# Performance work log

Measured on AMD Instinct MI355X. Metric: run time of the kernel, lower is better.

## Reference

```python
import jax, jax.numpy as jnp
import numpy as np

EPS = 1e-5


def _gn(v, axes, gamma, beta):
    # GroupNorm: normalize over `axes` per (batch, group), then affine.
    mu = jnp.mean(v, axis=axes, keepdims=True)
    var = jnp.var(v, axis=axes, keepdims=True)
    return (v - mu) * jax.lax.rsqrt(var + EPS) * gamma + beta


def setup_inputs() -> dict:
    key = jax.random.key(0)
    ks = jax.random.split(key, 5)
    B, G, BW, S, CD, H = 8, 32, 64, 64, 256, 64
    x = jax.random.normal(ks[0], (B, G * BW, H, H), jnp.float32)
    sent_embs = jax.random.normal(ks[1], (B, CD), jnp.float32)
    # grouped 1x1 conv weights stored as [group, out_per_group, in_per_group]
    Wq = jax.random.normal(ks[2], (G, S, CD), jnp.float32) * 0.05
    Wk = jax.random.normal(ks[3], (G, S, BW), jnp.float32) * 0.05
    Wv = jax.random.normal(ks[4], (G, S, BW), jnp.float32) * 0.05
    gamma1 = jnp.ones((G * S,), jnp.float32)
    beta1 = jnp.zeros((G * S,), jnp.float32)
    gamma2 = jnp.ones((G * S,), jnp.float32)
    beta2 = jnp.zeros((G * S,), jnp.float32)
    return {"x": x, "sent_embs": sent_embs, "Wq": Wq, "Wk": Wk, "Wv": Wv,
            "gamma1": gamma1, "beta1": beta1, "gamma2": gamma2, "beta2": beta2}


def reference(x, sent_embs, Wq, Wk, Wv, gamma1, beta1, gamma2, beta2):
    G, S, CD = Wq.shape
    B, C, H, W = x.shape
    BW = C // G
    xr = x.reshape(B, G, BW, H * W)                    # [B,G,bw,N]
    # query: same sent_emb broadcast to every group, grouped 1x1 conv
    q = jnp.einsum('bc,gsc->bgs', sent_embs, Wq)       # [B,G,S]
    q = _gn(q, (2,), gamma1.reshape(G, S), beta1.reshape(G, S))
    # key: grouped 1x1 conv over spatial map
    k = jnp.einsum('bgcn,gsc->bgsn', xr, Wk)           # [B,G,S,N]
    k = _gn(k, (2, 3), gamma2.reshape(G, S, 1), beta2.reshape(G, S, 1))
    # single-query attention per (batch, group)
    sim = jnp.einsum('bgs,bgsn->bgn', q, k)            # [B,G,N]
    attn = jax.nn.softmax(sim, axis=-1)
    out = jnp.einsum('bgn,bgcn->bgc', attn, xr)        # [B,G,bw]
    out = jnp.einsum('bgc,gsc->bgs', out, Wv)          # value grouped conv
    return out.reshape(B, G * S, 1, 1)
```

## Files before the change

### kernel.cpp

```cpp
#include <hip/hip_runtime.h>
#include <stdint.h>


#define EPS 1e-5f
#define NN 4096
#define NCHUNK 16
#define NSTR 264

typedef __bf16 bf16x8 __attribute__((ext_vector_type(8)));
typedef float f32x4 __attribute__((ext_vector_type(4)));

__global__ __launch_bounds__(64) void kA(const float* __restrict__ sent,
                                         const float* __restrict__ Wq,
                                         const float* __restrict__ Wk,
                                         const float* __restrict__ g1,
                                         const float* __restrict__ b1,
                                         const float* __restrict__ g2,
                                         float* __restrict__ w_all) {
  int bg = blockIdx.x; int b = bg >> 5; int g = bg & 31;
  int t = threadIdx.x;
  const float* wqrow = Wq + (size_t)(g * 64 + t) * 256;
  const float* se = sent + b * 256;
  float q = 0.f;
  for (int c = 0; c < 256; c += 4) {
    float4 wv = *(const float4*)(wqrow + c);
    q += se[c] * wv.x + se[c + 1] * wv.y + se[c + 2] * wv.z + se[c + 3] * wv.w;
  }
  float s = q;
  for (int off = 32; off; off >>= 1) s += __shfl_xor(s, off);
  float mu = s * (1.f / 64.f);
  float d = q - mu;
  float v = d * d;
  for (int off = 32; off; off >>= 1) v += __shfl_xor(v, off);
  float rsq = rsqrtf(v * (1.f / 64.f) + EPS);
  int gs = g * 64 + t;
  float qg2 = (d * rsq * g1[gs] + b1[gs]) * g2[gs];
  __shared__ float qs[64];
  qs[t] = qg2;
  __syncthreads();
  float wacc = 0.f;
  for (int s2 = 0; s2 < 64; s2++)
    wacc += qs[s2] * Wk[(size_t)(g * 64 + s2) * 64 + t];
  w_all[bg * 64 + t] = wacc;
}

__global__ __launch_bounds__(256) void kM(const float* __restrict__ Wk,
                                          float4* __restrict__ Mp,
                                          float* __restrict__ cw) {
  int g = blockIdx.x; int t = threadIdx.x;
  __shared__ float wk[4096];
  __shared__ float Ml[64 * 65];
  const float* wg = Wk + (size_t)g * 4096;
  #pragma unroll
  for (int i = 0; i < 16; i++) wk[t + 256 * i] = wg[t + 256 * i];
  __syncthreads();
  int c = t & 63, q = t >> 6;
  float acc[16];
  #pragma unroll
  for (int i = 0; i < 16; i++) acc[i] = 0.f;
  for (int s = 0; s < 64; s++) {
    float a = wk[s * 64 + c];
    const float* r = &wk[s * 64 + q * 16];
    #pragma unroll
    for (int i = 0; i < 16; i++) acc[i] += a * r[i];
  }
  #pragma unroll
  for (int i = 0; i < 16; i++) Ml[(q * 16 + i) * 65 + c] = acc[i];
  float s2 = 0.f;
  if (t < 64) {
    for (int s = 0; s < 64; s++) s2 += wk[s * 64 + t];
  }
  __syncthreads();
  if (t < 64) cw[g * 64 + t] = s2;
  int lane = t & 63, wv = t >> 6;
  int row = wv * 16 + ((lane >> 4) << 2);
  int col = lane & 15;
  #pragma unroll
  for (int r = 0; r < 4; r++) {
    float4 mv;
    mv.x = Ml[(row + 0) * 65 + r * 16 + col];
    mv.y = Ml[(row + 1) * 65 + r * 16 + col];
    mv.z = Ml[(row + 2) * 65 + r * 16 + col];
    mv.w = Ml[(row + 3) * 65 + r * 16 + col];
    Mp[(size_t)(g * 4 + r) * 256 + t] = mv;
  }
}

__global__ __launch_bounds__(256, 4) void kB(const float* __restrict__ x,
                                             const float* __restrict__ w_all,
                                             const float* __restrict__ cw,
                                             const float4* __restrict__ Mp,
                                             float* __restrict__ y_all,
                                             float* __restrict__ sums_part) {
  int bg = blockIdx.y; int b = bg >> 5; int g = bg & 31;
  int n0 = blockIdx.x * 256;
  int t = threadIdx.x;
  int lane = t & 63;
  int wv = t >> 6;

  __shared__ unsigned short xt[64 * NSTR];
  __shared__ float ypart[4 * 256];
  __shared__ float red[8];

  const float* wp = w_all + bg * 64 + wv * 16;
  const float* cwp = cw + g * 64 + wv * 16;
  float4 wq[4], cq[4];
  #pragma unroll
  for (int j = 0; j < 4; j++) { wq[j] = *(const float4*)(wp + j * 4); }
  #pragma unroll
  for (int j = 0; j < 4; j++) { cq[j] = *(const float4*)(cwp + j * 4); }

  const float* xb = x + ((size_t)(b * 2048 + g * 64 + wv * 16)) * NN + n0 + lane * 4;
  float4 v[16];
  #pragma unroll
  for (int k = 0; k < 16; k++) v[k] = *(const float4*)(xb + (size_t)k * NN);

  float y0 = 0, y1 = 0, y2 = 0, y3 = 0, zt = 0;
  unsigned short* xrow = &xt[(wv * 16) * NSTR + lane * 4];
  #pragma unroll
  for (int k = 0; k < 16; k++) {
    float wc = ((const float*)&wq[0])[k];
    float cc = ((const float*)&cq[0])[k];
    float4 vx = v[k];
    y0 += wc * vx.x; y1 += wc * vx.y; y2 += wc * vx.z; y3 += wc * vx.w;
    zt += cc * (vx.x + vx.y + vx.z + vx.w);
    unsigned a0 = __builtin_bit_cast(unsigned, vx.x) + 0x8000u;
    unsigned a1 = __builtin_bit_cast(unsigned, vx.y) + 0x8000u;
    unsigned a2 = __builtin_bit_cast(unsigned, vx.z) + 0x8000u;
    unsigned a3 = __builtin_bit_cast(unsigned, vx.w) + 0x8000u;
    uint2 pk;
    pk.x = (a0 >> 16) | (a1 & 0xffff0000u);
    pk.y = (a2 >> 16) | (a3 & 0xffff0000u);
    *(uint2*)(xrow + k * NSTR) = pk;
  }
  {
    float4 yp; yp.x = y0; yp.y = y1; yp.z = y2; yp.w = y3;
    *(float4*)&ypart[wv * 256 + lane * 4] = yp;
  }
  __syncthreads();
  y_all[(size_t)bg * NN + n0 + t] =
      ypart[t] + ypart[256 + t] + ypart[512 + t] + ypart[768 + t];

  int rbase = (lane & 15) * NSTR;
  int koff = (lane >> 4) * 8;
  int abase = (wv * 16 + (lane & 15)) * NSTR + koff;
  f32x4 acc[4];
  #pragma unroll
  for (int r = 0; r < 4; r++) acc[r] = (f32x4){0.f, 0.f, 0.f, 0.f};
  #pragma unroll
  for (int kk = 0; kk < 8; kk++) {
    uint4 au = *(const uint4*)&xt[abase + kk * 32];
    bf16x8 af = __builtin_bit_cast(bf16x8, au);
    #pragma unroll
    for (int r = 0; r < 4; r++) {
      uint4 bu = *(const uint4*)&xt[r * 16 * NSTR + rbase + kk * 32 + koff];
      bf16x8 bf = __builtin_bit_cast(bf16x8, bu);
      acc[r] = __builtin_amdgcn_mfma_f32_16x16x32_bf16(af, bf, acc[r], 0, 0, 0);
    }
  }
  float s2acc = 0.f;
  {
    const float4* mp = Mp + (size_t)g * 1024 + t;
    #pragma unroll
    for (int r = 0; r < 4; r++) {
      float4 mv = mp[r * 256];
      s2acc += acc[r][0] * mv.x + acc[r][1] * mv.y +
               acc[r][2] * mv.z + acc[r][3] * mv.w;
    }
  }
  for (int off = 32; off; off >>= 1) {
    zt += __shfl_xor(zt, off);
    s2acc += __shfl_xor(s2acc, off);
  }
  if (lane == 0) { red[wv] = zt; red[4 + wv] = s2acc; }
  __syncthreads();
  if (t == 0) {
    float* sp = sums_part + (size_t)(blockIdx.x * 256 + bg) * 2;
    sp[0] = red[0] + red[1] + red[2] + red[3];
    sp[1] = red[4] + red[5] + red[6] + red[7];
  }
}

__global__ __launch_bounds__(256) void kC(const float* __restrict__ y_all,
                                          const float* __restrict__ sums_part,
                                          float* __restrict__ attn) {
  int bg = blockIdx.x; int t = threadIdx.x;
  float s1 = 0.f, s2 = 0.f;
  for (int i = 0; i < NCHUNK; i++) {
    const float* sp = sums_part + (size_t)(i * 256 + bg) * 2;
    s1 += sp[0]; s2 += sp[1];
  }
  float mu = s1 * (1.f / 262144.f);
  float var = s2 * (1.f / 262144.f) - mu * mu;
  float rs = rsqrtf(var + EPS);
  const float* y = y_all + (size_t)bg * NN;
  float l[16];
  float m = -1e30f;
  #pragma unroll
  for (int i = 0; i < 16; i++) {
    l[i] = rs * y[t + 256 * i];
    m = fmaxf(m, l[i]);
  }
  __shared__ float red[8];
  for (int off = 32; off; off >>= 1) m = fmaxf(m, __shfl_xor(m, off));
  int wv = t >> 6, lane = t & 63;
  if (lane == 0) red[wv] = m;
  __syncthreads();
  m = fmaxf(fmaxf(red[0], red[1]), fmaxf(red[2], red[3]));
  float sum = 0.f;
  #pragma unroll
  for (int i = 0; i < 16; i++) { l[i] = __expf(l[i] - m); sum += l[i]; }
  for (int off = 32; off; off >>= 1) sum += __shfl_xor(sum, off);
  if (lane == 0) red[4 + wv] = sum;
  __syncthreads();
  float inv = 1.f / (red[4] + red[5] + red[6] + red[7]);
  float* ao = attn + (size_t)bg * NN;
  #pragma unroll
  for (int i = 0; i < 16; i++) ao[t + 256 * i] = l[i] * inv;
}

__global__ __launch_bounds__(256, 4) void kD(const float* __restrict__ x,
                                             const float* __restrict__ attn,
                                             float* __restrict__ outp) {
  int bg = 255 - blockIdx.y; int b = bg >> 5; int g = bg & 31;
  int n0 = (NCHUNK - 1 - blockIdx.x) * 256;
  int t = threadIdx.x; int lane = t & 63; int wv = t >> 6;
  float4 a = *(const float4*)(attn + (size_t)bg * NN + n0 + lane * 4);
  const float* xb = x + ((size_t)(b * 2048 + g * 64 + wv * 16)) * NN + n0 + lane * 4;
  float4 v[16];
  #pragma unroll
  for (int k = 0; k < 16; k++) v[k] = *(const float4*)(xb + (size_t)k * NN);
  float p[16];
  #pragma unroll
  for (int k = 0; k < 16; k++)
    p[k] = a.x * v[k].x + a.y * v[k].y + a.z * v[k].z + a.w * v[k].w;
  #pragma unroll
  for (int k = 0; k < 16; k++) {
    float r = p[k];
    for (int off = 32; off; off >>= 1) r += __shfl_xor(r, off);
    if (lane == 0)
      outp[(size_t)blockIdx.x * 16384 + bg * 64 + wv * 16 + k] = r;
  }
}

__global__ __launch_bounds__(64) void kE(const float* __restrict__ outp,
                                         const float* __restrict__ Wv,
                                         float* __restrict__ out) {
  int bg = blockIdx.x; int g = bg & 31;
  int t = threadIdx.x;
  __shared__ float oc[64];
  __shared__ float wvs[64 * 65];
  float s = 0.f;
  #pragma unroll
  for (int j = 0; j < NCHUNK; j++) s += outp[j * 16384 + bg * 64 + t];
  oc[t] = s;
  const float* wg = Wv + (size_t)g * 4096;
  for (int i = 0; i < 64; i++) wvs[i * 65 + t] = wg[i * 64 + t];
  __syncthreads();
  float acc = 0.f;
  for (int c = 0; c < 64; c++) acc += wvs[t * 65 + c] * oc[c];
  out[bg * 64 + t] = acc;
}

extern "C" void kernel_launch(void* const* d_in, const int* in_sizes, int n_in,
                              void* d_out, int out_size, void* d_ws, size_t ws_size,
                              hipStream_t stream) {
  const float* x    = (const float*)d_in[0];
  const float* sent = (const float*)d_in[1];
  const float* Wq   = (const float*)d_in[2];
  const float* Wk   = (const float*)d_in[3];
  const float* Wv   = (const float*)d_in[4];
  const float* g1   = (const float*)d_in[5];
  const float* b1   = (const float*)d_in[6];
  const float* g2   = (const float*)d_in[7];
  float* out = (float*)d_out;

  char* ws = (char*)d_ws;
  float*  w_all = (float*)(ws);
  float*  cw    = (float*)(ws + 65536);
  float4* Mp    = (float4*)(ws + 73728);
  float*  sumsp = (float*)(ws + 598016);
  float*  outp  = (float*)(ws + 630784);
  float*  y_all = (float*)(ws + 1679360);
  float*  attn  = (float*)(ws + 5873664);

  kA<<<256, 64, 0, stream>>>(sent, Wq, Wk, g1, b1, g2, w_all);
  kM<<<32, 256, 0, stream>>>(Wk, Mp, cw);
  kB<<<dim3(NCHUNK, 256), 256, 0, stream>>>(x, w_all, cw, Mp, y_all, sumsp);
  kC<<<256, 256, 0, stream>>>(y_all, sumsp, attn);
  kD<<<dim3(NCHUNK, 256), 256, 0, stream>>>(x, attn, outp);
  kE<<<256, 64, 0, stream>>>(outp, Wv, out);
}
```

Baseline: 433.2 us.

## Make kB and kD persistent over half-rows with register double-buffered loads

The streaming kernels kB and kD now launch 512 blocks instead of 4096. Each block walks eight 256-column chunks of half the spatial axis and prefetches the next chunk's x tile into a second register set while it computes the current one. kD walks its chunks in reverse to reuse cache from kB, and kC and kE reduce only two partials. This cuts launch and partial-reduction overhead and hides global load latency. In exchange it doubles register pressure (occupancy hint lowered to 2), adds two block syncs per chunk in kB, and leaves only 512 blocks to fill the GPU.

```diff
diff --git a/kernel.cpp b/kernel.cpp
--- a/kernel.cpp
+++ b/kernel.cpp
@@ -4,7 +4,6 @@
 
 #define EPS 1e-5f
 #define NN 4096
-#define NCHUNK 16
 #define NSTR 264
 
 typedef __bf16 bf16x8 __attribute__((ext_vector_type(8)));
@@ -86,17 +85,16 @@
   }
 }
 
-__global__ __launch_bounds__(256, 4) void kB(const float* __restrict__ x,
+__global__ __launch_bounds__(256, 2) void kB(const float* __restrict__ x,
                                              const float* __restrict__ w_all,
                                              const float* __restrict__ cw,
                                              const float4* __restrict__ Mp,
                                              float* __restrict__ y_all,
                                              float* __restrict__ sums_part) {
-  int bg = blockIdx.y; int b = bg >> 5; int g = bg & 31;
-  int n0 = blockIdx.x * 256;
-  int t = threadIdx.x;
-  int lane = t & 63;
-  int wv = t >> 6;
+  int bid = blockIdx.x;
+  int bg = bid >> 1, half = bid & 1;
+  int b = bg >> 5, g = bg & 31;
+  int t = threadIdx.x, lane = t & 63, wv = t >> 6;
 
   __shared__ unsigned short xt[64 * NSTR];
   __shared__ float ypart[4 * 256];
@@ -104,60 +102,72 @@
 
   const float* wp = w_all + bg * 64 + wv * 16;
   const float* cwp = cw + g * 64 + wv * 16;
-  float4 wq[4], cq[4];
-  #pragma unroll
-  for (int j = 0; j < 4; j++) { wq[j] = *(const float4*)(wp + j * 4); }
-  #pragma unroll
-  for (int j = 0; j < 4; j++) { cq[j] = *(const float4*)(cwp + j * 4); }
-
-  const float* xb = x + ((size_t)(b * 2048 + g * 64 + wv * 16)) * NN + n0 + lane * 4;
-  float4 v[16];
-  #pragma unroll
-  for (int k = 0; k < 16; k++) v[k] = *(const float4*)(xb + (size_t)k * NN);
-
-  float y0 = 0, y1 = 0, y2 = 0, y3 = 0, zt = 0;
+  const float* xb = x + ((size_t)(b * 2048 + g * 64 + wv * 16)) * NN +
+                    half * 2048 + lane * 4;
   unsigned short* xrow = &xt[(wv * 16) * NSTR + lane * 4];
-  #pragma unroll
-  for (int k = 0; k < 16; k++) {
-    float wc = ((const float*)&wq[0])[k];
-    float cc = ((const float*)&cq[0])[k];
-    float4 vx = v[k];
-    y0 += wc * vx.x; y1 += wc * vx.y; y2 += wc * vx.z; y3 += wc * vx.w;
-    zt += cc * (vx.x + vx.y + vx.z + vx.w);
-    unsigned a0 = __builtin_bit_cast(unsigned, vx.x) + 0x8000u;
-    unsigned a1 = __builtin_bit_cast(unsigned, vx.y) + 0x8000u;
-    unsigned a2 = __builtin_bit_cast(unsigned, vx.z) + 0x8000u;
-    unsigned a3 = __builtin_bit_cast(unsigned, vx.w) + 0x8000u;
-    uint2 pk;
-    pk.x = (a0 >> 16) | (a1 & 0xffff0000u);
-    pk.y = (a2 >> 16) | (a3 & 0xffff0000u);
-    *(uint2*)(xrow + k * NSTR) = pk;
-  }
-  {
-    float4 yp; yp.x = y0; yp.y = y1; yp.z = y2; yp.w = y3;
-    *(float4*)&ypart[wv * 256 + lane * 4] = yp;
-  }
-  __syncthreads();
-  y_all[(size_t)bg * NN + n0 + t] =
-      ypart[t] + ypart[256 + t] + ypart[512 + t] + ypart[768 + t];
 
   int rbase = (lane & 15) * NSTR;
   int koff = (lane >> 4) * 8;
   int abase = (wv * 16 + (lane & 15)) * NSTR + koff;
+
+  float zt = 0.f;
   f32x4 acc[4];
   #pragma unroll
   for (int r = 0; r < 4; r++) acc[r] = (f32x4){0.f, 0.f, 0.f, 0.f};
-  #pragma unroll
-  for (int kk = 0; kk < 8; kk++) {
-    uint4 au = *(const uint4*)&xt[abase + kk * 32];
-    bf16x8 af = __builtin_bit_cast(bf16x8, au);
-    #pragma unroll
-    for (int r = 0; r < 4; r++) {
-      uint4 bu = *(const uint4*)&xt[r * 16 * NSTR + rbase + kk * 32 + koff];
-      bf16x8 bf = __builtin_bit_cast(bf16x8, bu);
-      acc[r] = __builtin_amdgcn_mfma_f32_16x16x32_bf16(af, bf, acc[r], 0, 0, 0);
-    }
-  }
+
+  float4 v0[16], v1[16];
+  #pragma unroll
+  for (int k = 0; k < 16; k++) v0[k] = *(const float4*)(xb + (size_t)k * NN);
+
+  auto stepB = [&](int i, float4 (&cur)[16], float4 (&nxt)[16]) {
+    if (i < 7) {
+      const float* xn = xb + (size_t)(i + 1) * 256;
+      #pragma unroll
+      for (int k = 0; k < 16; k++) nxt[k] = *(const float4*)(xn + (size_t)k * NN);
+    }
+    float y0 = 0, y1 = 0, y2 = 0, y3 = 0;
+    uint2 pk[16];
+    #pragma unroll
+    for (int k = 0; k < 16; k++) {
+      float wc = wp[k], cc = cwp[k];
+      float4 vx = cur[k];
+      y0 += wc * vx.x; y1 += wc * vx.y; y2 += wc * vx.z; y3 += wc * vx.w;
+      zt += cc * (vx.x + vx.y + vx.z + vx.w);
+      unsigned a0 = __builtin_bit_cast(unsigned, vx.x) + 0x8000u;
+      unsigned a1 = __builtin_bit_cast(unsigned, vx.y) + 0x8000u;
+      unsigned a2 = __builtin_bit_cast(unsigned, vx.z) + 0x8000u;
+      unsigned a3 = __builtin_bit_cast(unsigned, vx.w) + 0x8000u;
+      pk[k].x = (a0 >> 16) | (a1 & 0xffff0000u);
+      pk[k].y = (a2 >> 16) | (a3 & 0xffff0000u);
+    }
+    __syncthreads();
+    #pragma unroll
+    for (int k = 0; k < 16; k++) *(uint2*)(xrow + k * NSTR) = pk[k];
+    {
+      float4 yp; yp.x = y0; yp.y = y1; yp.z = y2; yp.w = y3;
+      *(float4*)&ypart[wv * 256 + lane * 4] = yp;
+    }
+    __syncthreads();
+    y_all[(size_t)bg * NN + half * 2048 + i * 256 + t] =
+        ypart[t] + ypart[256 + t] + ypart[512 + t] + ypart[768 + t];
+    #pragma unroll
+    for (int kk = 0; kk < 8; kk++) {
+      uint4 au = *(const uint4*)&xt[abase + kk * 32];
+      bf16x8 af = __builtin_bit_cast(bf16x8, au);
+      #pragma unroll
+      for (int r = 0; r < 4; r++) {
+        uint4 bu = *(const uint4*)&xt[r * 16 * NSTR + rbase + kk * 32 + koff];
+        bf16x8 bf = __builtin_bit_cast(bf16x8, bu);
+        acc[r] = __builtin_amdgcn_mfma_f32_16x16x32_bf16(af, bf, acc[r], 0, 0, 0);
+      }
+    }
+  };
+  #pragma unroll
+  for (int ii = 0; ii < 8; ii += 2) {
+    stepB(ii, v0, v1);
+    stepB(ii + 1, v1, v0);
+  }
+
   float s2acc = 0.f;
   {
     const float4* mp = Mp + (size_t)g * 1024 + t;
@@ -175,7 +185,7 @@
   if (lane == 0) { red[wv] = zt; red[4 + wv] = s2acc; }
   __syncthreads();
   if (t == 0) {
-    float* sp = sums_part + (size_t)(blockIdx.x * 256 + bg) * 2;
+    float* sp = sums_part + (size_t)(half * 256 + bg) * 2;
     sp[0] = red[0] + red[1] + red[2] + red[3];
     sp[1] = red[4] + red[5] + red[6] + red[7];
   }
@@ -186,7 +196,7 @@
                                           float* __restrict__ attn) {
   int bg = blockIdx.x; int t = threadIdx.x;
   float s1 = 0.f, s2 = 0.f;
-  for (int i = 0; i < NCHUNK; i++) {
+  for (int i = 0; i < 2; i++) {
     const float* sp = sums_part + (size_t)(i * 256 + bg) * 2;
     s1 += sp[0]; s2 += sp[1];
   }
@@ -219,27 +229,51 @@
   for (int i = 0; i < 16; i++) ao[t + 256 * i] = l[i] * inv;
 }
 
-__global__ __launch_bounds__(256, 4) void kD(const float* __restrict__ x,
+__global__ __launch_bounds__(256, 2) void kD(const float* __restrict__ x,
                                              const float* __restrict__ attn,
                                              float* __restrict__ outp) {
-  int bg = 255 - blockIdx.y; int b = bg >> 5; int g = bg & 31;
-  int n0 = (NCHUNK - 1 - blockIdx.x) * 256;
-  int t = threadIdx.x; int lane = t & 63; int wv = t >> 6;
-  float4 a = *(const float4*)(attn + (size_t)bg * NN + n0 + lane * 4);
-  const float* xb = x + ((size_t)(b * 2048 + g * 64 + wv * 16)) * NN + n0 + lane * 4;
-  float4 v[16];
-  #pragma unroll
-  for (int k = 0; k < 16; k++) v[k] = *(const float4*)(xb + (size_t)k * NN);
+  int bid = blockIdx.x;
+  int bg = bid >> 1, half = bid & 1;
+  int b = bg >> 5, g = bg & 31;
+  int t = threadIdx.x, lane = t & 63, wv = t >> 6;
+  const float* xb = x + ((size_t)(b * 2048 + g * 64 + wv * 16)) * NN +
+                    half * 2048 + lane * 4;
+  const float* ab = attn + (size_t)bg * NN + half * 2048 + lane * 4;
+
   float p[16];
   #pragma unroll
-  for (int k = 0; k < 16; k++)
-    p[k] = a.x * v[k].x + a.y * v[k].y + a.z * v[k].z + a.w * v[k].w;
+  for (int k = 0; k < 16; k++) p[k] = 0.f;
+
+  float4 v0[16], v1[16], a0, a1;
+  {
+    const float* xn = xb + (size_t)7 * 256;
+    a0 = *(const float4*)(ab + 7 * 256);
+    #pragma unroll
+    for (int k = 0; k < 16; k++) v0[k] = *(const float4*)(xn + (size_t)k * NN);
+  }
+  auto stepD = [&](int i, float4 (&cur)[16], float4& ac,
+                   float4 (&nxt)[16], float4& an) {
+    if (i > 0) {
+      const float* xn = xb + (size_t)(i - 1) * 256;
+      an = *(const float4*)(ab + (i - 1) * 256);
+      #pragma unroll
+      for (int k = 0; k < 16; k++) nxt[k] = *(const float4*)(xn + (size_t)k * NN);
+    }
+    #pragma unroll
+    for (int k = 0; k < 16; k++)
+      p[k] += ac.x * cur[k].x + ac.y * cur[k].y +
+              ac.z * cur[k].z + ac.w * cur[k].w;
+  };
+  #pragma unroll
+  for (int ii = 0; ii < 8; ii += 2) {
+    stepD(7 - ii, v0, a0, v1, a1);
+    stepD(6 - ii, v1, a1, v0, a0);
+  }
   #pragma unroll
   for (int k = 0; k < 16; k++) {
     float r = p[k];
     for (int off = 32; off; off >>= 1) r += __shfl_xor(r, off);
-    if (lane == 0)
-      outp[(size_t)blockIdx.x * 16384 + bg * 64 + wv * 16 + k] = r;
+    if (lane == 0) outp[(size_t)half * 16384 + bg * 64 + wv * 16 + k] = r;
   }
 }
 
@@ -250,10 +284,7 @@
   int t = threadIdx.x;
   __shared__ float oc[64];
   __shared__ float wvs[64 * 65];
-  float s = 0.f;
-  #pragma unroll
-  for (int j = 0; j < NCHUNK; j++) s += outp[j * 16384 + bg * 64 + t];
-  oc[t] = s;
+  oc[t] = outp[bg * 64 + t] + outp[16384 + bg * 64 + t];
   const float* wg = Wv + (size_t)g * 4096;
   for (int i = 0; i < 64; i++) wvs[i * 65 + t] = wg[i * 64 + t];
   __syncthreads();
@@ -280,14 +311,14 @@
   float*  cw    = (float*)(ws + 65536);
   float4* Mp    = (float4*)(ws + 73728);
   float*  sumsp = (float*)(ws + 598016);
-  float*  outp  = (float*)(ws + 630784);
-  float*  y_all = (float*)(ws + 1679360);
-  float*  attn  = (float*)(ws + 5873664);
+  float*  outp  = (float*)(ws + 602112);
+  float*  y_all = (float*)(ws + 733184);
+  float*  attn  = (float*)(ws + 4927488);
 
   kA<<<256, 64, 0, stream>>>(sent, Wq, Wk, g1, b1, g2, w_all);
   kM<<<32, 256, 0, stream>>>(Wk, Mp, cw);
-  kB<<<dim3(NCHUNK, 256), 256, 0, stream>>>(x, w_all, cw, Mp, y_all, sumsp);
+  kB<<<512, 256, 0, stream>>>(x, w_all, cw, Mp, y_all, sumsp);
   kC<<<256, 256, 0, stream>>>(y_all, sumsp, attn);
-  kD<<<dim3(NCHUNK, 256), 256, 0, stream>>>(x, attn, outp);
+  kD<<<512, 256, 0, stream>>>(x, attn, outp);
   kE<<<256, 64, 0, stream>>>(outp, Wv, out);
 }
```

New measurement: 531.9 us. 1.23x slower.

## Stage x tiles via direct global-to-LDS loads in kB/kD and widen small kernels

Applied to the files above, without the earlier changes.

kB and kD now copy their 64x256 fp32 x tile straight into shared memory with global_load_lds instead of going through registers. kB computes the y and z projections from shared memory and converts to bf16 on the fly for the MFMA Gram product. kD computes the attention-weighted sums from the shared tile and reduces them in shared memory instead of with 16 shuffle reductions. kA and kE are widened to 256 threads with split-K partial sums. The larger fp32 shared tile lowers occupancy (launch bounds drop to 2 blocks per CU) in exchange for fewer register round trips and shuffles.

```diff
diff --git a/kernel.cpp b/kernel.cpp
--- a/kernel.cpp
+++ b/kernel.cpp
@@ -4,44 +4,75 @@
 
 #define EPS 1e-5f
 #define NN 4096
-#define NCHUNK 16
-#define NSTR 264
+#define XSTR 268
 
 typedef __bf16 bf16x8 __attribute__((ext_vector_type(8)));
 typedef float f32x4 __attribute__((ext_vector_type(4)));
 
-__global__ __launch_bounds__(64) void kA(const float* __restrict__ sent,
-                                         const float* __restrict__ Wq,
-                                         const float* __restrict__ Wk,
-                                         const float* __restrict__ g1,
-                                         const float* __restrict__ b1,
-                                         const float* __restrict__ g2,
-                                         float* __restrict__ w_all) {
+__device__ __forceinline__ void gload16(const float* g, float* l) {
+  __builtin_amdgcn_global_load_lds(
+      (const __attribute__((address_space(1))) unsigned int*)g,
+      (__attribute__((address_space(3))) unsigned int*)l, 16, 0, 0);
+}
+
+__device__ __forceinline__ bf16x8 cvt8(float4 a, float4 b) {
+  unsigned u0 = __builtin_bit_cast(unsigned, a.x) + 0x8000u;
+  unsigned u1 = __builtin_bit_cast(unsigned, a.y) + 0x8000u;
+  unsigned u2 = __builtin_bit_cast(unsigned, a.z) + 0x8000u;
+  unsigned u3 = __builtin_bit_cast(unsigned, a.w) + 0x8000u;
+  unsigned u4 = __builtin_bit_cast(unsigned, b.x) + 0x8000u;
+  unsigned u5 = __builtin_bit_cast(unsigned, b.y) + 0x8000u;
+  unsigned u6 = __builtin_bit_cast(unsigned, b.z) + 0x8000u;
+  unsigned u7 = __builtin_bit_cast(unsigned, b.w) + 0x8000u;
+  uint4 r;
+  r.x = (u0 >> 16) | (u1 & 0xffff0000u);
+  r.y = (u2 >> 16) | (u3 & 0xffff0000u);
+  r.z = (u4 >> 16) | (u5 & 0xffff0000u);
+  r.w = (u6 >> 16) | (u7 & 0xffff0000u);
+  return __builtin_bit_cast(bf16x8, r);
+}
+
+__global__ __launch_bounds__(256) void kA(const float* __restrict__ sent,
+                                          const float* __restrict__ Wq,
+                                          const float* __restrict__ Wk,
+                                          const float* __restrict__ g1,
+                                          const float* __restrict__ b1,
+                                          const float* __restrict__ g2,
+                                          float* __restrict__ w_all) {
   int bg = blockIdx.x; int b = bg >> 5; int g = bg & 31;
-  int t = threadIdx.x;
-  const float* wqrow = Wq + (size_t)(g * 64 + t) * 256;
-  const float* se = sent + b * 256;
-  float q = 0.f;
-  for (int c = 0; c < 256; c += 4) {
-    float4 wv = *(const float4*)(wqrow + c);
-    q += se[c] * wv.x + se[c + 1] * wv.y + se[c + 2] * wv.z + se[c + 3] * wv.w;
-  }
-  float s = q;
-  for (int off = 32; off; off >>= 1) s += __shfl_xor(s, off);
-  float mu = s * (1.f / 64.f);
-  float d = q - mu;
-  float v = d * d;
-  for (int off = 32; off; off >>= 1) v += __shfl_xor(v, off);
-  float rsq = rsqrtf(v * (1.f / 64.f) + EPS);
-  int gs = g * 64 + t;
-  float qg2 = (d * rsq * g1[gs] + b1[gs]) * g2[gs];
-  __shared__ float qs[64];
-  qs[t] = qg2;
-  __syncthreads();
-  float wacc = 0.f;
-  for (int s2 = 0; s2 < 64; s2++)
-    wacc += qs[s2] * Wk[(size_t)(g * 64 + s2) * 64 + t];
-  w_all[bg * 64 + t] = wacc;
+  int t = threadIdx.x, lane = t & 63, wv = t >> 6;
+  __shared__ float qp[256], qs[64], wpp[256];
+  const float* se = sent + b * 256 + wv * 64;
+  const float* wqrow = Wq + (size_t)(g * 64 + lane) * 256 + wv * 64;
+  float acc = 0.f;
+  #pragma unroll
+  for (int c = 0; c < 64; c += 4) {
+    float4 w4 = *(const float4*)(wqrow + c);
+    acc += se[c] * w4.x + se[c + 1] * w4.y + se[c + 2] * w4.z + se[c + 3] * w4.w;
+  }
+  qp[wv * 64 + lane] = acc;
+  __syncthreads();
+  if (wv == 0) {
+    float q = qp[lane] + qp[64 + lane] + qp[128 + lane] + qp[192 + lane];
+    float s = q;
+    for (int off = 32; off; off >>= 1) s += __shfl_xor(s, off);
+    float mu = s * (1.f / 64.f);
+    float d = q - mu;
+    float v = d * d;
+    for (int off = 32; off; off >>= 1) v += __shfl_xor(v, off);
+    float rsq = rsqrtf(v * (1.f / 64.f) + EPS);
+    int gs = g * 64 + lane;
+    qs[lane] = (d * rsq * g1[gs] + b1[gs]) * g2[gs];
+  }
+  __syncthreads();
+  const float* wkb = Wk + (size_t)(g * 64 + wv * 16) * 64 + lane;
+  float wa = 0.f;
+  #pragma unroll
+  for (int s2 = 0; s2 < 16; s2++) wa += qs[wv * 16 + s2] * wkb[s2 * 64];
+  wpp[wv * 64 + lane] = wa;
+  __syncthreads();
+  if (wv == 0)
+    w_all[bg * 64 + lane] = wpp[lane] + wpp[64 + lane] + wpp[128 + lane] + wpp[192 + lane];
 }
 
 __global__ __launch_bounds__(256) void kM(const float* __restrict__ Wk,
@@ -86,76 +117,54 @@
   }
 }
 
-__global__ __launch_bounds__(256, 4) void kB(const float* __restrict__ x,
+__global__ __launch_bounds__(256, 2) void kB(const float* __restrict__ x,
                                              const float* __restrict__ w_all,
                                              const float* __restrict__ cw,
                                              const float4* __restrict__ Mp,
                                              float* __restrict__ y_all,
                                              float* __restrict__ sums_part) {
-  int bg = blockIdx.y; int b = bg >> 5; int g = bg & 31;
-  int n0 = blockIdx.x * 256;
-  int t = threadIdx.x;
-  int lane = t & 63;
-  int wv = t >> 6;
-
-  __shared__ unsigned short xt[64 * NSTR];
-  __shared__ float ypart[4 * 256];
+  int bid = blockIdx.x;
+  int bg = bid >> 4, ch = bid & 15;
+  int b = bg >> 5, g = bg & 31;
+  int t = threadIdx.x, lane = t & 63, wv = t >> 6;
+  int n0 = ch * 256;
+
+  __shared__ float xt[64 * XSTR];
+  __shared__ float wl[64], cwl[64];
   __shared__ float red[8];
 
-  const float* wp = w_all + bg * 64 + wv * 16;
-  const float* cwp = cw + g * 64 + wv * 16;
-  float4 wq[4], cq[4];
-  #pragma unroll
-  for (int j = 0; j < 4; j++) { wq[j] = *(const float4*)(wp + j * 4); }
-  #pragma unroll
-  for (int j = 0; j < 4; j++) { cq[j] = *(const float4*)(cwp + j * 4); }
-
-  const float* xb = x + ((size_t)(b * 2048 + g * 64 + wv * 16)) * NN + n0 + lane * 4;
-  float4 v[16];
-  #pragma unroll
-  for (int k = 0; k < 16; k++) v[k] = *(const float4*)(xb + (size_t)k * NN);
-
-  float y0 = 0, y1 = 0, y2 = 0, y3 = 0, zt = 0;
-  unsigned short* xrow = &xt[(wv * 16) * NSTR + lane * 4];
-  #pragma unroll
-  for (int k = 0; k < 16; k++) {
-    float wc = ((const float*)&wq[0])[k];
-    float cc = ((const float*)&cq[0])[k];
-    float4 vx = v[k];
-    y0 += wc * vx.x; y1 += wc * vx.y; y2 += wc * vx.z; y3 += wc * vx.w;
-    zt += cc * (vx.x + vx.y + vx.z + vx.w);
-    unsigned a0 = __builtin_bit_cast(unsigned, vx.x) + 0x8000u;
-    unsigned a1 = __builtin_bit_cast(unsigned, vx.y) + 0x8000u;
-    unsigned a2 = __builtin_bit_cast(unsigned, vx.z) + 0x8000u;
-    unsigned a3 = __builtin_bit_cast(unsigned, vx.w) + 0x8000u;
-    uint2 pk;
-    pk.x = (a0 >> 16) | (a1 & 0xffff0000u);
-    pk.y = (a2 >> 16) | (a3 & 0xffff0000u);
-    *(uint2*)(xrow + k * NSTR) = pk;
-  }
-  {
-    float4 yp; yp.x = y0; yp.y = y1; yp.z = y2; yp.w = y3;
-    *(float4*)&ypart[wv * 256 + lane * 4] = yp;
-  }
-  __syncthreads();
-  y_all[(size_t)bg * NN + n0 + t] =
-      ypart[t] + ypart[256 + t] + ypart[512 + t] + ypart[768 + t];
-
-  int rbase = (lane & 15) * NSTR;
-  int koff = (lane >> 4) * 8;
-  int abase = (wv * 16 + (lane & 15)) * NSTR + koff;
+  if (t < 64) { wl[t] = w_all[bg * 64 + t]; cwl[t] = cw[g * 64 + t]; }
+
+  const float* xrow = x + ((size_t)(b * 2048 + g * 64 + wv * 16)) * NN + n0 + lane * 4;
+  #pragma unroll
+  for (int k = 0; k < 16; k++)
+    gload16(xrow + (size_t)k * NN, &xt[(wv * 16 + k) * XSTR]);
+  __syncthreads();
+
+  float y = 0.f, z = 0.f;
+  #pragma unroll 8
+  for (int c = 0; c < 64; c++) {
+    float v = xt[c * XSTR + t];
+    y += wl[c] * v;
+    z += cwl[c] * v;
+  }
+  y_all[(size_t)bg * NN + n0 + t] = y;
+
+  int rbase = (lane & 15) * XSTR + (lane >> 4) * 8;
+  int abase = (wv * 16 + (lane & 15)) * XSTR + (lane >> 4) * 8;
   f32x4 acc[4];
   #pragma unroll
   for (int r = 0; r < 4; r++) acc[r] = (f32x4){0.f, 0.f, 0.f, 0.f};
   #pragma unroll
   for (int kk = 0; kk < 8; kk++) {
-    uint4 au = *(const uint4*)&xt[abase + kk * 32];
-    bf16x8 af = __builtin_bit_cast(bf16x8, au);
+    float4 a0 = *(const float4*)&xt[abase + kk * 32];
+    float4 a1 = *(const float4*)&xt[abase + kk * 32 + 4];
+    bf16x8 af = cvt8(a0, a1);
     #pragma unroll
     for (int r = 0; r < 4; r++) {
-      uint4 bu = *(const uint4*)&xt[r * 16 * NSTR + rbase + kk * 32 + koff];
-      bf16x8 bf = __builtin_bit_cast(bf16x8, bu);
-      acc[r] = __builtin_amdgcn_mfma_f32_16x16x32_bf16(af, bf, acc[r], 0, 0, 0);
+      float4 b0 = *(const float4*)&xt[r * 16 * XSTR + rbase + kk * 32];
+      float4 b1 = *(const float4*)&xt[r * 16 * XSTR + rbase + kk * 32 + 4];
+      acc[r] = __builtin_amdgcn_mfma_f32_16x16x32_bf16(af, cvt8(b0, b1), acc[r], 0, 0, 0);
     }
   }
   float s2acc = 0.f;
@@ -169,13 +178,13 @@
     }
   }
   for (int off = 32; off; off >>= 1) {
-    zt += __shfl_xor(zt, off);
+    z += __shfl_xor(z, off);
     s2acc += __shfl_xor(s2acc, off);
   }
-  if (lane == 0) { red[wv] = zt; red[4 + wv] = s2acc; }
+  if (lane == 0) { red[wv] = z; red[4 + wv] = s2acc; }
   __syncthreads();
   if (t == 0) {
-    float* sp = sums_part + (size_t)(blockIdx.x * 256 + bg) * 2;
+    float* sp = sums_part + (size_t)(ch * 256 + bg) * 2;
     sp[0] = red[0] + red[1] + red[2] + red[3];
     sp[1] = red[4] + red[5] + red[6] + red[7];
   }
@@ -186,7 +195,7 @@
                                           float* __restrict__ attn) {
   int bg = blockIdx.x; int t = threadIdx.x;
   float s1 = 0.f, s2 = 0.f;
-  for (int i = 0; i < NCHUNK; i++) {
+  for (int i = 0; i < 16; i++) {
     const float* sp = sums_part + (size_t)(i * 256 + bg) * 2;
     s1 += sp[0]; s2 += sp[1];
   }
@@ -219,47 +228,70 @@
   for (int i = 0; i < 16; i++) ao[t + 256 * i] = l[i] * inv;
 }
 
-__global__ __launch_bounds__(256, 4) void kD(const float* __restrict__ x,
+__global__ __launch_bounds__(256, 2) void kD(const float* __restrict__ x,
                                              const float* __restrict__ attn,
                                              float* __restrict__ outp) {
-  int bg = 255 - blockIdx.y; int b = bg >> 5; int g = bg & 31;
-  int n0 = (NCHUNK - 1 - blockIdx.x) * 256;
-  int t = threadIdx.x; int lane = t & 63; int wv = t >> 6;
-  float4 a = *(const float4*)(attn + (size_t)bg * NN + n0 + lane * 4);
-  const float* xb = x + ((size_t)(b * 2048 + g * 64 + wv * 16)) * NN + n0 + lane * 4;
-  float4 v[16];
-  #pragma unroll
-  for (int k = 0; k < 16; k++) v[k] = *(const float4*)(xb + (size_t)k * NN);
-  float p[16];
+  int bid = blockIdx.x;
+  int bg = 255 - (bid >> 4), ch = 15 - (bid & 15);
+  int b = bg >> 5, g = bg & 31;
+  int t = threadIdx.x, lane = t & 63, wv = t >> 6;
+  int n0 = ch * 256;
+
+  __shared__ float xt[64 * XSTR];
+  __shared__ float al[256];
+  __shared__ float pp[256];
+
+  const float* xrow = x + ((size_t)(b * 2048 + g * 64 + wv * 16)) * NN + n0 + lane * 4;
+  if (wv == 0) gload16(attn + (size_t)bg * NN + n0 + lane * 4, al);
   #pragma unroll
   for (int k = 0; k < 16; k++)
-    p[k] = a.x * v[k].x + a.y * v[k].y + a.z * v[k].z + a.w * v[k].w;
-  #pragma unroll
-  for (int k = 0; k < 16; k++) {
-    float r = p[k];
-    for (int off = 32; off; off >>= 1) r += __shfl_xor(r, off);
-    if (lane == 0)
-      outp[(size_t)blockIdx.x * 16384 + bg * 64 + wv * 16 + k] = r;
-  }
-}
-
-__global__ __launch_bounds__(64) void kE(const float* __restrict__ outp,
-                                         const float* __restrict__ Wv,
-                                         float* __restrict__ out) {
+    gload16(xrow + (size_t)k * NN, &xt[(wv * 16 + k) * XSTR]);
+  __syncthreads();
+
+  float p = 0.f;
+  const float* xr = &xt[lane * XSTR + wv * 64];
+  const float* ar = &al[wv * 64];
+  #pragma unroll
+  for (int j = 0; j < 64; j += 4) {
+    float4 xv = *(const float4*)(xr + j);
+    p += ar[j] * xv.x + ar[j + 1] * xv.y + ar[j + 2] * xv.z + ar[j + 3] * xv.w;
+  }
+  pp[wv * 64 + lane] = p;
+  __syncthreads();
+  if (t < 64)
+    outp[(size_t)ch * 16384 + bg * 64 + t] =
+        pp[t] + pp[64 + t] + pp[128 + t] + pp[192 + t];
+}
+
+__global__ __launch_bounds__(256) void kE(const float* __restrict__ outp,
+                                          const float* __restrict__ Wv,
+                                          float* __restrict__ out) {
   int bg = blockIdx.x; int g = bg & 31;
-  int t = threadIdx.x;
+  int t = threadIdx.x, lane = t & 63, wv = t >> 6;
   __shared__ float oc[64];
   __shared__ float wvs[64 * 65];
-  float s = 0.f;
-  #pragma unroll
-  for (int j = 0; j < NCHUNK; j++) s += outp[j * 16384 + bg * 64 + t];
-  oc[t] = s;
+  __shared__ float ep[256];
+  if (t < 64) {
+    float s = 0.f;
+    #pragma unroll
+    for (int j = 0; j < 16; j++) s += outp[j * 16384 + bg * 64 + t];
+    oc[t] = s;
+  }
   const float* wg = Wv + (size_t)g * 4096;
-  for (int i = 0; i < 64; i++) wvs[i * 65 + t] = wg[i * 64 + t];
+  #pragma unroll
+  for (int i = 0; i < 16; i++) {
+    int idx = i * 256 + t;
+    wvs[(idx >> 6) * 65 + (idx & 63)] = wg[idx];
+  }
   __syncthreads();
   float acc = 0.f;
-  for (int c = 0; c < 64; c++) acc += wvs[t * 65 + c] * oc[c];
-  out[bg * 64 + t] = acc;
+  #pragma unroll
+  for (int j = 0; j < 16; j++)
+    acc += wvs[lane * 65 + wv * 16 + j] * oc[wv * 16 + j];
+  ep[wv * 64 + lane] = acc;
+  __syncthreads();
+  if (wv == 0)
+    out[bg * 64 + lane] = ep[lane] + ep[64 + lane] + ep[128 + lane] + ep[192 + lane];
 }
 
 extern "C" void kernel_launch(void* const* d_in, const int* in_sizes, int n_in,
@@ -284,10 +316,10 @@
   float*  y_all = (float*)(ws + 1679360);
   float*  attn  = (float*)(ws + 5873664);
 
-  kA<<<256, 64, 0, stream>>>(sent, Wq, Wk, g1, b1, g2, w_all);
+  kA<<<256, 256, 0, stream>>>(sent, Wq, Wk, g1, b1, g2, w_all);
   kM<<<32, 256, 0, stream>>>(Wk, Mp, cw);
-  kB<<<dim3(NCHUNK, 256), 256, 0, stream>>>(x, w_all, cw, Mp, y_all, sumsp);
+  kB<<<4096, 256, 0, stream>>>(x, w_all, cw, Mp, y_all, sumsp);
   kC<<<256, 256, 0, stream>>>(y_all, sumsp, attn);
-  kD<<<dim3(NCHUNK, 256), 256, 0, stream>>>(x, attn, outp);
-  kE<<<256, 64, 0, stream>>>(outp, Wv, out);
-}
+  kD<<<4096, 256, 0, stream>>>(x, attn, outp);
+  kE<<<256, 256, 0, stream>>>(outp, Wv, out);
+}
```

Measured after the change: 422.2 us. 2.6% less time.
